# Kernel optimization log

Measured on AMD Instinct MI355X. Metric: run time of the kernel, lower is better.

## Reference

```python
import jax, jax.numpy as jnp
import numpy as np

N_NODES = 50000
N_EDGES = 600000
N_ELEMENTS = 100
N_RBF = 50
D = 128
CUTOFF = 5.0


def setup_inputs() -> dict:
    key = jax.random.key(0)
    ks = jax.random.split(key, 10)
    node_type = jax.random.randint(ks[0], (N_NODES,), 0, N_ELEMENTS)
    x_nodes = jax.random.normal(ks[1], (N_NODES, D), dtype=jnp.float32)
    src = jax.random.randint(ks[2], (N_EDGES,), 0, N_NODES)
    dst = jax.random.randint(ks[3], (N_EDGES,), 0, N_NODES)
    rbf_edges = jax.random.normal(ks[4], (N_EDGES, N_RBF), dtype=jnp.float32)
    dist = jax.random.uniform(ks[5], (N_EDGES,), dtype=jnp.float32) * (CUTOFF * 1.2)
    emb = jax.random.normal(ks[6], (N_ELEMENTS, D), dtype=jnp.float32) * 0.1
    W_e = jax.random.normal(ks[7], (D, N_RBF), dtype=jnp.float32) * (1.0 / np.sqrt(N_RBF))
    b_e = jnp.zeros((D,), dtype=jnp.float32)
    W_c = jax.random.normal(ks[8], (D, 2 * D), dtype=jnp.float32) * (1.0 / np.sqrt(2 * D))
    b_c = jnp.zeros((D,), dtype=jnp.float32)
    return {"node_type": node_type, "x_nodes": x_nodes, "src": src, "dst": dst,
            "rbf_edges": rbf_edges, "dist": dist, "emb": emb,
            "W_e": W_e, "b_e": b_e, "W_c": W_c, "b_c": b_c}


def cosine_cutoff(dist, cutoff):
    # 0.5*(cos(pi*d/cutoff)+1), zeroed beyond cutoff
    w = 0.5 * (jnp.cos(dist * (jnp.pi / cutoff)) + 1.0)
    return w * (dist < cutoff).astype(dist.dtype)


def reference(node_type, x_nodes, src, dst, rbf_edges, dist, emb, W_e, b_e, W_c, b_c):
    # node embedding from atom type: [N, D]
    x_neighbors = emb[node_type]
    # edge projection weighted by cutoff: [E, D]
    x_edges = (rbf_edges @ W_e.T + b_e) * cosine_cutoff(dist, CUTOFF)[:, None]
    # gather source node embedding, multiply by edge embedding, scatter-sum to dst
    msg = x_neighbors[src] * x_edges  # [E, D]
    x_integrated = jax.ops.segment_sum(msg, dst, num_segments=N_NODES)  # [N, D]
    # concat + combine linear: [N, D]
    x_combine = jnp.concatenate([x_nodes, x_integrated], axis=-1)
    return x_combine @ W_c.T + b_c
```

## Files before the change

kernel.cpp:

```cpp
#include <hip/hip_runtime.h>
#include <hip/hip_bf16.h>

constexpr int NN   = 50000;
constexpr int NE   = 600000;
constexpr int NRBF = 50;
constexpr int DIM  = 128;
constexpr float CUT = 5.0f;
constexpr float PI_F = 3.14159265358979323846f;

constexpr int CAP = 32;

constexpr size_t OFF_DEG   = 0;
constexpr size_t OFF_OVFC  = (size_t)NN * 4;
constexpr size_t OFF_EID   = 200960;
constexpr size_t OFF_OVF   = OFF_EID  + (size_t)NN * CAP * 4;
constexpr size_t OFF_CC    = OFF_OVF  + (size_t)NE * 4;
constexpr size_t OFF_EROW  = OFF_CC   + (size_t)NE * 4;
constexpr size_t OFF_WAUG  = OFF_EROW + (size_t)NE * 4;
constexpr size_t OFF_EPERM = OFF_WAUG + 128 * 64 * 2;
constexpr size_t OFF_MSG   = 13843200;
constexpr size_t OFF_XI    = OFF_MSG  + (size_t)NE * DIM * 2;


typedef __attribute__((ext_vector_type(4))) float f32x4;
typedef __attribute__((ext_vector_type(8))) short short8;

__device__ __forceinline__ float bf2f(unsigned short u) {
    return __uint_as_float(((unsigned int)u) << 16);
}
__device__ __forceinline__ unsigned short f2bf(float f) {
    return __bfloat16_as_ushort(__float2bfloat16(f));
}

__global__ __launch_bounds__(256)
void prep_w(const float* __restrict__ W_e, const float* __restrict__ b_e,
            const float* __restrict__ emb,
            unsigned short* __restrict__ W_aug, unsigned short* __restrict__ emb_perm)
{
    const int tid = blockIdx.x * 256 + threadIdx.x;
    if (tid < 128 * 64) {
        const int d = tid >> 6, k = tid & 63;
        float v = 0.0f;
        if (k < NRBF)       v = W_e[d * NRBF + k];
        else if (k == NRBF) v = b_e[d];
        W_aug[tid] = f2bf(v);
    } else if (tid < 128 * 64 + 100 * 128) {
        const int i = tid - 128 * 64;
        const int tau = i >> 7, p = i & 127;
        const int d = 16 * (p & 7) + (p >> 3);
        emb_perm[i] = f2bf(emb[tau * DIM + d]);
    }
}

__global__ __launch_bounds__(256)
void build_buckets(const int* __restrict__ dst, const float* __restrict__ dist,
                   const int* __restrict__ src, const int* __restrict__ node_type,
                   int* __restrict__ deg, int* __restrict__ eid,
                   int* __restrict__ ovf, int* __restrict__ ovf_cnt,
                   float* __restrict__ cc_arr, int* __restrict__ embrow)
{
    const int e = blockIdx.x * 256 + threadIdx.x;
    if (e >= NE) return;
    const float dd = dist[e];
    const bool act = dd < CUT;
    const float w = 0.5f * (__cosf(dd * (PI_F / CUT)) + 1.0f);
    cc_arr[e] = act ? w : 0.0f;
    embrow[e] = act ? node_type[src[e]] : -1;
    if (act) {
        const int n = dst[e];
        const int pos = atomicAdd(&deg[n], 1);
        if (pos < CAP) eid[n * CAP + pos] = e;
        else           ovf[atomicAdd(ovf_cnt, 1)] = e;
    }
}

__global__ __launch_bounds__(256)
void edge_msg_reg(const float* __restrict__ rbf,
                  const float* __restrict__ cc_arr,
                  const int* __restrict__ embrow,
                  const unsigned short* __restrict__ W_aug,
                  const unsigned short* __restrict__ emb_perm,
                  unsigned short* __restrict__ msg)
{
    const int t  = threadIdx.x;
    const int wv = t >> 6, l = t & 63;
    const int c  = l & 15, g = l >> 4;

    short8 bfrag[16];
    #pragma unroll
    for (int nt = 0; nt < 8; ++nt)
        #pragma unroll
        for (int s = 0; s < 2; ++s)
            bfrag[nt * 2 + s] =
                *(const short8*)(W_aug + (nt * 16 + c) * 64 + s * 32 + g * 8);

    #pragma unroll
    for (int tile = 0; tile < 4; ++tile) {
        const int e0 = (blockIdx.x * 4 + tile) * 64;
        if (e0 < NE) {
            const int er = e0 + wv * 16 + c;
            const float ccl = cc_arr[er];
            const float* rp = rbf + (size_t)er * NRBF;

            int erow[4];
            #pragma unroll
            for (int r = 0; r < 4; ++r)
                erow[r] = embrow[e0 + wv * 16 + 4 * g + r];

            const float2 r0 = *(const float2*)(rp + 8 * g);
            const float2 r1 = *(const float2*)(rp + 8 * g + 2);
            const float2 r2 = *(const float2*)(rp + 8 * g + 4);
            const float2 r3 = *(const float2*)(rp + 8 * g + 6);
            float2 q0 = make_float2(0.f, 0.f), q1 = q0, q2 = q0, q3 = q0;
            if (g < 2) {
                q0 = *(const float2*)(rp + 32 + 8 * g);
                q1 = *(const float2*)(rp + 32 + 8 * g + 2);
                q2 = *(const float2*)(rp + 32 + 8 * g + 4);
                q3 = *(const float2*)(rp + 32 + 8 * g + 6);
            } else if (g == 2) {
                q0 = *(const float2*)(rp + 48);
            }

            short8 a0, a1;
            a0[0] = (short)f2bf(ccl * r0.x); a0[1] = (short)f2bf(ccl * r0.y);
            a0[2] = (short)f2bf(ccl * r1.x); a0[3] = (short)f2bf(ccl * r1.y);
            a0[4] = (short)f2bf(ccl * r2.x); a0[5] = (short)f2bf(ccl * r2.y);
            a0[6] = (short)f2bf(ccl * r3.x); a0[7] = (short)f2bf(ccl * r3.y);
            a1[0] = (short)f2bf(ccl * q0.x); a1[1] = (short)f2bf(ccl * q0.y);
            a1[2] = (short)f2bf(ccl * q1.x); a1[3] = (short)f2bf(ccl * q1.y);
            a1[4] = (short)f2bf(ccl * q2.x); a1[5] = (short)f2bf(ccl * q2.y);
            a1[6] = (short)f2bf(ccl * q3.x); a1[7] = (short)f2bf(ccl * q3.y);
            if (g == 2) {
                a1[2] = (short)f2bf(ccl);
                a1[3] = 0; a1[4] = 0; a1[5] = 0; a1[6] = 0; a1[7] = 0;
            }

            f32x4 acc[8] = {};
            #pragma unroll
            for (int nt = 0; nt < 8; ++nt)
                acc[nt] = __builtin_amdgcn_mfma_f32_16x16x32_bf16(a0, bfrag[nt * 2],
                                                                  acc[nt], 0, 0, 0);
            #pragma unroll
            for (int nt = 0; nt < 8; ++nt)
                acc[nt] = __builtin_amdgcn_mfma_f32_16x16x32_bf16(a1, bfrag[nt * 2 + 1],
                                                                  acc[nt], 0, 0, 0);

            #pragma unroll
            for (int r = 0; r < 4; ++r) {
                const int e = e0 + wv * 16 + 4 * g + r;
                const int rw = erow[r];
                if (rw >= 0) {
                    const int4 em = *(const int4*)(emb_perm + rw * DIM + 8 * c);
                    const unsigned int* ep = (const unsigned int*)&em;
                    unsigned int ow[4];
                    #pragma unroll
                    for (int q = 0; q < 4; ++q) {
                        const float m0 = bf2f((unsigned short)(ep[q] & 0xffff));
                        const float m1 = bf2f((unsigned short)(ep[q] >> 16));
                        const float v0 = acc[2 * q][r] * m0;
                        const float v1 = acc[2 * q + 1][r] * m1;
                        ow[q] = (unsigned int)f2bf(v0) | ((unsigned int)f2bf(v1) << 16);
                    }
                    *(int4*)(msg + (size_t)e * DIM + 8 * c) =
                        make_int4((int)ow[0], (int)ow[1], (int)ow[2], (int)ow[3]);
                }
            }
        }
    }
}

__global__ __launch_bounds__(256)
void gather_sum(const unsigned short* __restrict__ msg, const int* __restrict__ deg,
                const int* __restrict__ eid, const int* __restrict__ ovf,
                const int* __restrict__ ovf_cnt, const int* __restrict__ dst,
                unsigned short* __restrict__ xi)
{
    const int t = threadIdx.x, l = t & 63;
    const int c = l & 15, g = l >> 4;
    const int n = blockIdx.x * 4 + (t >> 6);
    if (n >= NN) return;

    const int dn   = deg[n];
    const int degn = dn < CAP ? dn : CAP;
    int eidv = 0;
    if (l < degn) eidv = eid[n * CAP + l];

    float v[8] = {};
    for (int j = 0; j < degn; j += 4) {
        const int e = __shfl(eidv, j + g);
        if (j + g < degn) {
            const int4 mv = *(const int4*)(msg + (size_t)e * DIM + 8 * c);
            const unsigned int* mp = (const unsigned int*)&mv;
            #pragma unroll
            for (int q = 0; q < 4; ++q) {
                v[2 * q]     += bf2f((unsigned short)(mp[q] & 0xffff));
                v[2 * q + 1] += bf2f((unsigned short)(mp[q] >> 16));
            }
        }
    }
    const int ocnt = ovf_cnt[0];
    for (int j = 0; j < ocnt; ++j) {
        const int e = ovf[j];
        if (g == 0 && dst[e] == n) {
            const int4 mv = *(const int4*)(msg + (size_t)e * DIM + 8 * c);
            const unsigned int* mp = (const unsigned int*)&mv;
            #pragma unroll
            for (int q = 0; q < 4; ++q) {
                v[2 * q]     += bf2f((unsigned short)(mp[q] & 0xffff));
                v[2 * q + 1] += bf2f((unsigned short)(mp[q] >> 16));
            }
        }
    }

    #pragma unroll
    for (int q = 0; q < 8; ++q) {
        v[q] += __shfl_xor(v[q], 16);
        v[q] += __shfl_xor(v[q], 32);
    }

    float s0 = v[0], s1 = v[1];
    if (g == 1)      { s0 = v[2]; s1 = v[3]; }
    else if (g == 2) { s0 = v[4]; s1 = v[5]; }
    else if (g == 3) { s0 = v[6]; s1 = v[7]; }
    xi[(size_t)n * DIM + 32 * g + c]      = f2bf(s0);
    xi[(size_t)n * DIM + 32 * g + 16 + c] = f2bf(s1);
}

__global__ __launch_bounds__(256)
void combine_mfma(const float* __restrict__ x_nodes, const __hip_bfloat16* __restrict__ xi,
                  const float* __restrict__ W_c, const float* __restrict__ b_c,
                  float* __restrict__ out)
{
    __shared__ unsigned short As[64][72];
    __shared__ unsigned short Bs[128][72];

    const int t  = threadIdx.x;
    const int wv = t >> 6;
    const int l  = t & 63;
    const int n0 = blockIdx.x * 64;

    f32x4 acc[8] = {};

    for (int kc = 0; kc < 4; ++kc) {
        const int kb = kc * 64;
        if (kc) __syncthreads();
        {
            const int r  = t >> 2;
            const int c0 = (t & 3) * 16;
            const int n  = n0 + r;
            if (kc < 2) {
                float4 v[4];
                if (n < NN) {
                    const float4* p = (const float4*)(x_nodes + (size_t)n * DIM + kb + c0);
                    v[0] = p[0]; v[1] = p[1]; v[2] = p[2]; v[3] = p[3];
                } else {
                    v[0] = v[1] = v[2] = v[3] = make_float4(0.f, 0.f, 0.f, 0.f);
                }
                unsigned short* dp = &As[r][c0];
                #pragma unroll
                for (int q = 0; q < 4; ++q) {
                    *(ushort2*)&dp[q * 4]     = make_ushort2(f2bf(v[q].x), f2bf(v[q].y));
                    *(ushort2*)&dp[q * 4 + 2] = make_ushort2(f2bf(v[q].z), f2bf(v[q].w));
                }
            } else {
                int4 v0 = make_int4(0, 0, 0, 0), v1 = make_int4(0, 0, 0, 0);
                if (n < NN) {
                    const int4* p = (const int4*)(xi + (size_t)n * DIM + (kb - DIM) + c0);
                    v0 = p[0];
                    v1 = p[1];
                }
                *(int4*)&As[r][c0]     = v0;
                *(int4*)&As[r][c0 + 8] = v1;
            }
        }
        {
            const int dch = t >> 1;
            const int c0  = (t & 1) * 32;
            const float4* p = (const float4*)(W_c + (size_t)dch * (2 * DIM) + kb + c0);
            unsigned short* dp = &Bs[dch][c0];
            #pragma unroll
            for (int q = 0; q < 8; ++q) {
                const float4 v = p[q];
                *(ushort2*)&dp[q * 4]     = make_ushort2(f2bf(v.x), f2bf(v.y));
                *(ushort2*)&dp[q * 4 + 2] = make_ushort2(f2bf(v.z), f2bf(v.w));
            }
        }
        __syncthreads();
        #pragma unroll
        for (int s = 0; s < 2; ++s) {
            const int ko = s * 32 + (l >> 4) * 8;
            const short8 af = *(const short8*)&As[wv * 16 + (l & 15)][ko];
            #pragma unroll
            for (int nt = 0; nt < 8; ++nt) {
                const short8 bf = *(const short8*)&Bs[nt * 16 + (l & 15)][ko];
                acc[nt] = __builtin_amdgcn_mfma_f32_16x16x32_bf16(af, bf, acc[nt], 0, 0, 0);
            }
        }
    }

    const int col = l & 15;
    const int rq  = (l >> 4) * 4;
    #pragma unroll
    for (int nt = 0; nt < 8; ++nt) {
        const int dim = nt * 16 + col;
        const float bc = b_c[dim];
        #pragma unroll
        for (int r = 0; r < 4; ++r) {
            const int node = n0 + wv * 16 + rq + r;
            if (node < NN)
                out[(size_t)node * DIM + dim] = acc[nt][r] + bc;
        }
    }
}

extern "C" void kernel_launch(void* const* d_in, const int* in_sizes, int n_in,
                              void* d_out, int out_size, void* d_ws, size_t ws_size,
                              hipStream_t stream)
{
    const int*   node_type = (const int*)  d_in[0];
    const float* x_nodes   = (const float*)d_in[1];
    const int*   src       = (const int*)  d_in[2];
    const int*   dst       = (const int*)  d_in[3];
    const float* rbf       = (const float*)d_in[4];
    const float* dist      = (const float*)d_in[5];
    const float* emb       = (const float*)d_in[6];
    const float* W_e       = (const float*)d_in[7];
    const float* b_e       = (const float*)d_in[8];
    const float* W_c       = (const float*)d_in[9];
    const float* b_c       = (const float*)d_in[10];
    float* out = (float*)d_out;

    char* ws = (char*)d_ws;
    int*            deg      = (int*)(ws + OFF_DEG);
    int*            ovf_cnt  = (int*)(ws + OFF_OVFC);
    int*            eid      = (int*)(ws + OFF_EID);
    int*            ovf      = (int*)(ws + OFF_OVF);
    float*          cc_arr   = (float*)(ws + OFF_CC);
    int*            embrow   = (int*)(ws + OFF_EROW);
    unsigned short* W_aug    = (unsigned short*)(ws + OFF_WAUG);
    unsigned short* emb_perm = (unsigned short*)(ws + OFF_EPERM);
    unsigned short* msg      = (unsigned short*)(ws + OFF_MSG);
    unsigned short* xi       = (unsigned short*)(ws + OFF_XI);

    hipMemsetAsync(deg, 0, (NN + 1) * sizeof(int), stream);

    prep_w<<<82, 256, 0, stream>>>(W_e, b_e, emb, W_aug, emb_perm);

    build_buckets<<<(NE + 255) / 256, 256, 0, stream>>>(
        dst, dist, src, node_type, deg, eid, ovf, ovf_cnt, cc_arr, embrow);

    edge_msg_reg<<<(NE / 64 + 3) / 4, 256, 0, stream>>>(
        rbf, cc_arr, embrow, W_aug, emb_perm, msg);

    gather_sum<<<(NN + 3) / 4, 256, 0, stream>>>(msg, deg, eid, ovf, ovf_cnt, dst, xi);

    combine_mfma<<<(NN + 63) / 64, 256, 0, stream>>>(
        x_nodes, (const __hip_bfloat16*)xi, W_c, b_c, out);
}
```

Before: 356.9 us.

## Double-buffer rbf tiles into LDS via async global_load_lds in edge kernel

```diff
diff --git a/kernel.cpp b/kernel.cpp
--- a/kernel.cpp
+++ b/kernel.cpp
@@ -9,6 +9,7 @@
 constexpr float PI_F = 3.14159265358979323846f;
 
 constexpr int CAP = 32;
+constexpr int NTILES = NE / 64;
 
 constexpr size_t OFF_DEG   = 0;
 constexpr size_t OFF_OVFC  = (size_t)NN * 4;
@@ -74,14 +75,32 @@
     }
 }
 
-__global__ __launch_bounds__(256)
-void edge_msg_reg(const float* __restrict__ rbf,
+__device__ __forceinline__ void stage_rbf(const float* __restrict__ rbf, int tt,
+                                          void* lds_base, int wv, int l)
+{
+    const char* gb = (const char*)rbf + (size_t)tt * 12800 + (size_t)wv * 3200;
+    char* lb = (char*)lds_base + wv * 3200;
+    #pragma unroll
+    for (int i = 0; i < 4; ++i) {
+        if (i * 64 + l < 200) {
+            __builtin_amdgcn_global_load_lds(
+                (const __attribute__((address_space(1))) unsigned int*)(gb + (size_t)(i * 64 + l) * 16),
+                (__attribute__((address_space(3))) unsigned int*)(lb + i * 1024),
+                16, 0, 0);
+        }
+    }
+}
+
+__global__ __launch_bounds__(256)
+void edge_msg_lds(const float* __restrict__ rbf,
                   const float* __restrict__ cc_arr,
                   const int* __restrict__ embrow,
                   const unsigned short* __restrict__ W_aug,
                   const unsigned short* __restrict__ emb_perm,
                   unsigned short* __restrict__ msg)
 {
+    __shared__ __align__(16) float sbuf[2][3200];
+
     const int t  = threadIdx.x;
     const int wv = t >> 6, l = t & 63;
     const int c  = l & 15, g = l >> 4;
@@ -94,31 +113,43 @@
             bfrag[nt * 2 + s] =
                 *(const short8*)(W_aug + (nt * 16 + c) * 64 + s * 32 + g * 8);
 
+    const int tt0 = blockIdx.x * 4;
+
+    stage_rbf(rbf, tt0, (void*)sbuf[0], wv, l);
+
     #pragma unroll
     for (int tile = 0; tile < 4; ++tile) {
-        const int e0 = (blockIdx.x * 4 + tile) * 64;
-        if (e0 < NE) {
+        const int tt = tt0 + tile;
+
+        if (tile < 3 && tt + 1 < NTILES) {
+            stage_rbf(rbf, tt + 1, (void*)sbuf[(tile + 1) & 1], wv, l);
+            asm volatile("s_waitcnt vmcnt(4)" ::: "memory");
+        } else {
+            asm volatile("s_waitcnt vmcnt(0)" ::: "memory");
+        }
+
+        if (tt < NTILES) {
+            const int e0 = tt * 64;
             const int er = e0 + wv * 16 + c;
             const float ccl = cc_arr[er];
-            const float* rp = rbf + (size_t)er * NRBF;
-
-            int erow[4];
-            #pragma unroll
-            for (int r = 0; r < 4; ++r)
-                erow[r] = embrow[e0 + wv * 16 + 4 * g + r];
-
-            const float2 r0 = *(const float2*)(rp + 8 * g);
-            const float2 r1 = *(const float2*)(rp + 8 * g + 2);
-            const float2 r2 = *(const float2*)(rp + 8 * g + 4);
-            const float2 r3 = *(const float2*)(rp + 8 * g + 6);
+
+            const int4 er4 = *(const int4*)(embrow + e0 + wv * 16 + 4 * g);
+            const int* erow = (const int*)&er4;
+
+            const float2* rp2 =
+                (const float2*)((const char*)sbuf[tile & 1] + (wv * 16 + c) * 200);
+            const float2 r0 = rp2[4 * g];
+            const float2 r1 = rp2[4 * g + 1];
+            const float2 r2 = rp2[4 * g + 2];
+            const float2 r3 = rp2[4 * g + 3];
             float2 q0 = make_float2(0.f, 0.f), q1 = q0, q2 = q0, q3 = q0;
             if (g < 2) {
-                q0 = *(const float2*)(rp + 32 + 8 * g);
-                q1 = *(const float2*)(rp + 32 + 8 * g + 2);
-                q2 = *(const float2*)(rp + 32 + 8 * g + 4);
-                q3 = *(const float2*)(rp + 32 + 8 * g + 6);
+                q0 = rp2[16 + 4 * g];
+                q1 = rp2[17 + 4 * g];
+                q2 = rp2[18 + 4 * g];
+                q3 = rp2[19 + 4 * g];
             } else if (g == 2) {
-                q0 = *(const float2*)(rp + 48);
+                q0 = rp2[24];
             }
 
             short8 a0, a1;
@@ -349,7 +380,7 @@
     build_buckets<<<(NE + 255) / 256, 256, 0, stream>>>(
         dst, dist, src, node_type, deg, eid, ovf, ovf_cnt, cc_arr, embrow);
 
-    edge_msg_reg<<<(NE / 64 + 3) / 4, 256, 0, stream>>>(
+    edge_msg_lds<<<(NTILES + 3) / 4, 256, 0, stream>>>(
         rbf, cc_arr, embrow, W_aug, emb_perm, msg);
 
     gather_sum<<<(NN + 3) / 4, 256, 0, stream>>>(msg, deg, eid, ovf, ovf_cnt, dst, xi);
```

Result: no change. 356.5 us (-0.1%).

## Fuse edge message MFMA into per-destination gather, dropping the msg buffer

Applied to the files above, without the earlier changes.

```diff
diff --git a/kernel.cpp b/kernel.cpp
--- a/kernel.cpp
+++ b/kernel.cpp
@@ -13,13 +13,12 @@
 constexpr size_t OFF_DEG   = 0;
 constexpr size_t OFF_OVFC  = (size_t)NN * 4;
 constexpr size_t OFF_EID   = 200960;
-constexpr size_t OFF_OVF   = OFF_EID  + (size_t)NN * CAP * 4;
-constexpr size_t OFF_CC    = OFF_OVF  + (size_t)NE * 4;
-constexpr size_t OFF_EROW  = OFF_CC   + (size_t)NE * 4;
-constexpr size_t OFF_WAUG  = OFF_EROW + (size_t)NE * 4;
+constexpr size_t OFF_CCB   = OFF_EID  + (size_t)NN * CAP * 4;
+constexpr size_t OFF_TAUB  = OFF_CCB  + (size_t)NN * CAP * 4;
+constexpr size_t OFF_OVF   = OFF_TAUB + (size_t)NN * CAP * 4;
+constexpr size_t OFF_WAUG  = OFF_OVF  + (size_t)NE * 4;
 constexpr size_t OFF_EPERM = OFF_WAUG + 128 * 64 * 2;
-constexpr size_t OFF_MSG   = 13843200;
-constexpr size_t OFF_XI    = OFF_MSG  + (size_t)NE * DIM * 2;
+constexpr size_t OFF_XI    = OFF_EPERM + 100 * 128 * 2;
 
 
 typedef __attribute__((ext_vector_type(4))) float f32x4;
@@ -56,158 +55,139 @@
 void build_buckets(const int* __restrict__ dst, const float* __restrict__ dist,
                    const int* __restrict__ src, const int* __restrict__ node_type,
                    int* __restrict__ deg, int* __restrict__ eid,
-                   int* __restrict__ ovf, int* __restrict__ ovf_cnt,
-                   float* __restrict__ cc_arr, int* __restrict__ embrow)
+                   float* __restrict__ ccb, int* __restrict__ taub,
+                   int* __restrict__ ovf, int* __restrict__ ovf_cnt)
 {
     const int e = blockIdx.x * 256 + threadIdx.x;
     if (e >= NE) return;
     const float dd = dist[e];
-    const bool act = dd < CUT;
+    if (dd >= CUT) return;
     const float w = 0.5f * (__cosf(dd * (PI_F / CUT)) + 1.0f);
-    cc_arr[e] = act ? w : 0.0f;
-    embrow[e] = act ? node_type[src[e]] : -1;
-    if (act) {
-        const int n = dst[e];
-        const int pos = atomicAdd(&deg[n], 1);
-        if (pos < CAP) eid[n * CAP + pos] = e;
-        else           ovf[atomicAdd(ovf_cnt, 1)] = e;
+    const int n = dst[e];
+    const int pos = atomicAdd(&deg[n], 1);
+    if (pos < CAP) {
+        eid[n * CAP + pos]  = e;
+        ccb[n * CAP + pos]  = w;
+        taub[n * CAP + pos] = node_type[src[e]];
+    } else {
+        ovf[atomicAdd(ovf_cnt, 1)] = e;
     }
 }
 
 __global__ __launch_bounds__(256)
-void edge_msg_reg(const float* __restrict__ rbf,
-                  const float* __restrict__ cc_arr,
-                  const int* __restrict__ embrow,
+void gather_fused(const float* __restrict__ rbf,
+                  const int* __restrict__ deg, const int* __restrict__ eid,
+                  const float* __restrict__ ccb, const int* __restrict__ taub,
                   const unsigned short* __restrict__ W_aug,
                   const unsigned short* __restrict__ emb_perm,
-                  unsigned short* __restrict__ msg)
-{
-    const int t  = threadIdx.x;
-    const int wv = t >> 6, l = t & 63;
-    const int c  = l & 15, g = l >> 4;
-
-    short8 bfrag[16];
-    #pragma unroll
-    for (int nt = 0; nt < 8; ++nt)
-        #pragma unroll
-        for (int s = 0; s < 2; ++s)
-            bfrag[nt * 2 + s] =
-                *(const short8*)(W_aug + (nt * 16 + c) * 64 + s * 32 + g * 8);
-
-    #pragma unroll
-    for (int tile = 0; tile < 4; ++tile) {
-        const int e0 = (blockIdx.x * 4 + tile) * 64;
-        if (e0 < NE) {
-            const int er = e0 + wv * 16 + c;
-            const float ccl = cc_arr[er];
-            const float* rp = rbf + (size_t)er * NRBF;
-
-            int erow[4];
-            #pragma unroll
-            for (int r = 0; r < 4; ++r)
-                erow[r] = embrow[e0 + wv * 16 + 4 * g + r];
-
-            const float2 r0 = *(const float2*)(rp + 8 * g);
-            const float2 r1 = *(const float2*)(rp + 8 * g + 2);
-            const float2 r2 = *(const float2*)(rp + 8 * g + 4);
-            const float2 r3 = *(const float2*)(rp + 8 * g + 6);
-            float2 q0 = make_float2(0.f, 0.f), q1 = q0, q2 = q0, q3 = q0;
-            if (g < 2) {
-                q0 = *(const float2*)(rp + 32 + 8 * g);
-                q1 = *(const float2*)(rp + 32 + 8 * g + 2);
-                q2 = *(const float2*)(rp + 32 + 8 * g + 4);
-                q3 = *(const float2*)(rp + 32 + 8 * g + 6);
-            } else if (g == 2) {
-                q0 = *(const float2*)(rp + 48);
-            }
-
-            short8 a0, a1;
-            a0[0] = (short)f2bf(ccl * r0.x); a0[1] = (short)f2bf(ccl * r0.y);
-            a0[2] = (short)f2bf(ccl * r1.x); a0[3] = (short)f2bf(ccl * r1.y);
-            a0[4] = (short)f2bf(ccl * r2.x); a0[5] = (short)f2bf(ccl * r2.y);
-            a0[6] = (short)f2bf(ccl * r3.x); a0[7] = (short)f2bf(ccl * r3.y);
-            a1[0] = (short)f2bf(ccl * q0.x); a1[1] = (short)f2bf(ccl * q0.y);
-            a1[2] = (short)f2bf(ccl * q1.x); a1[3] = (short)f2bf(ccl * q1.y);
-            a1[4] = (short)f2bf(ccl * q2.x); a1[5] = (short)f2bf(ccl * q2.y);
-            a1[6] = (short)f2bf(ccl * q3.x); a1[7] = (short)f2bf(ccl * q3.y);
-            if (g == 2) {
-                a1[2] = (short)f2bf(ccl);
-                a1[3] = 0; a1[4] = 0; a1[5] = 0; a1[6] = 0; a1[7] = 0;
-            }
-
-            f32x4 acc[8] = {};
-            #pragma unroll
-            for (int nt = 0; nt < 8; ++nt)
-                acc[nt] = __builtin_amdgcn_mfma_f32_16x16x32_bf16(a0, bfrag[nt * 2],
-                                                                  acc[nt], 0, 0, 0);
-            #pragma unroll
-            for (int nt = 0; nt < 8; ++nt)
-                acc[nt] = __builtin_amdgcn_mfma_f32_16x16x32_bf16(a1, bfrag[nt * 2 + 1],
-                                                                  acc[nt], 0, 0, 0);
-
-            #pragma unroll
-            for (int r = 0; r < 4; ++r) {
-                const int e = e0 + wv * 16 + 4 * g + r;
-                const int rw = erow[r];
-                if (rw >= 0) {
-                    const int4 em = *(const int4*)(emb_perm + rw * DIM + 8 * c);
-                    const unsigned int* ep = (const unsigned int*)&em;
-                    unsigned int ow[4];
-                    #pragma unroll
-                    for (int q = 0; q < 4; ++q) {
-                        const float m0 = bf2f((unsigned short)(ep[q] & 0xffff));
-                        const float m1 = bf2f((unsigned short)(ep[q] >> 16));
-                        const float v0 = acc[2 * q][r] * m0;
-                        const float v1 = acc[2 * q + 1][r] * m1;
-                        ow[q] = (unsigned int)f2bf(v0) | ((unsigned int)f2bf(v1) << 16);
-                    }
-                    *(int4*)(msg + (size_t)e * DIM + 8 * c) =
-                        make_int4((int)ow[0], (int)ow[1], (int)ow[2], (int)ow[3]);
-                }
-            }
-        }
-    }
-}
-
-__global__ __launch_bounds__(256)
-void gather_sum(const unsigned short* __restrict__ msg, const int* __restrict__ deg,
-                const int* __restrict__ eid, const int* __restrict__ ovf,
-                const int* __restrict__ ovf_cnt, const int* __restrict__ dst,
-                unsigned short* __restrict__ xi)
+                  const int* __restrict__ ovf, const int* __restrict__ ovf_cnt,
+                  const int* __restrict__ dst, const float* __restrict__ dist,
+                  const int* __restrict__ src, const int* __restrict__ node_type,
+                  unsigned short* __restrict__ xi)
 {
     const int t = threadIdx.x, l = t & 63;
     const int c = l & 15, g = l >> 4;
     const int n = blockIdx.x * 4 + (t >> 6);
     if (n >= NN) return;
 
+    short8 bfrag[16];
+    #pragma unroll
+    for (int nt = 0; nt < 8; ++nt)
+        #pragma unroll
+        for (int s = 0; s < 2; ++s)
+            bfrag[nt * 2 + s] =
+                *(const short8*)(W_aug + (nt * 16 + c) * 64 + s * 32 + g * 8);
+
     const int dn   = deg[n];
     const int degn = dn < CAP ? dn : CAP;
-    int eidv = 0;
-    if (l < degn) eidv = eid[n * CAP + l];
+    const int base = n * CAP;
 
     float v[8] = {};
-    for (int j = 0; j < degn; j += 4) {
-        const int e = __shfl(eidv, j + g);
-        if (j + g < degn) {
-            const int4 mv = *(const int4*)(msg + (size_t)e * DIM + 8 * c);
-            const unsigned int* mp = (const unsigned int*)&mv;
-            #pragma unroll
-            for (int q = 0; q < 4; ++q) {
-                v[2 * q]     += bf2f((unsigned short)(mp[q] & 0xffff));
-                v[2 * q + 1] += bf2f((unsigned short)(mp[q] >> 16));
-            }
-        }
-    }
+
+    for (int j0 = 0; j0 < degn; j0 += 16) {
+        const int slot = j0 + c;
+        int   ea  = 0;
+        float ccl = 0.0f;
+        if (slot < degn) {
+            ea  = eid[base + slot];
+            ccl = ccb[base + slot];
+        }
+        const float* rp = rbf + (size_t)ea * NRBF;
+
+        const float2* rp2 = (const float2*)rp;
+        const float2 r0 = rp2[4 * g];
+        const float2 r1 = rp2[4 * g + 1];
+        const float2 r2 = rp2[4 * g + 2];
+        const float2 r3 = rp2[4 * g + 3];
+        float2 q0 = make_float2(0.f, 0.f), q1 = q0, q2 = q0, q3 = q0;
+        if (g < 2) {
+            q0 = rp2[16 + 4 * g];
+            q1 = rp2[17 + 4 * g];
+            q2 = rp2[18 + 4 * g];
+            q3 = rp2[19 + 4 * g];
+        } else if (g == 2) {
+            q0 = rp2[24];
+        }
+
+        short8 a0, a1;
+        a0[0] = (short)f2bf(ccl * r0.x); a0[1] = (short)f2bf(ccl * r0.y);
+        a0[2] = (short)f2bf(ccl * r1.x); a0[3] = (short)f2bf(ccl * r1.y);
+        a0[4] = (short)f2bf(ccl * r2.x); a0[5] = (short)f2bf(ccl * r2.y);
+        a0[6] = (short)f2bf(ccl * r3.x); a0[7] = (short)f2bf(ccl * r3.y);
+        a1[0] = (short)f2bf(ccl * q0.x); a1[1] = (short)f2bf(ccl * q0.y);
+        a1[2] = (short)f2bf(ccl * q1.x); a1[3] = (short)f2bf(ccl * q1.y);
+        a1[4] = (short)f2bf(ccl * q2.x); a1[5] = (short)f2bf(ccl * q2.y);
+        a1[6] = (short)f2bf(ccl * q3.x); a1[7] = (short)f2bf(ccl * q3.y);
+        if (g == 2) {
+            a1[2] = (short)f2bf(ccl);
+            a1[3] = 0; a1[4] = 0; a1[5] = 0; a1[6] = 0; a1[7] = 0;
+        }
+
+        f32x4 acc[8] = {};
+        #pragma unroll
+        for (int nt = 0; nt < 8; ++nt)
+            acc[nt] = __builtin_amdgcn_mfma_f32_16x16x32_bf16(a0, bfrag[nt * 2],
+                                                              acc[nt], 0, 0, 0);
+        #pragma unroll
+        for (int nt = 0; nt < 8; ++nt)
+            acc[nt] = __builtin_amdgcn_mfma_f32_16x16x32_bf16(a1, bfrag[nt * 2 + 1],
+                                                              acc[nt], 0, 0, 0);
+
+        #pragma unroll
+        for (int r = 0; r < 4; ++r) {
+            const int jr = j0 + 4 * g + r;
+            if (jr < degn) {
+                const int rw = taub[base + jr];
+                const int4 em = *(const int4*)(emb_perm + rw * DIM + 8 * c);
+                const unsigned int* ep = (const unsigned int*)&em;
+                #pragma unroll
+                for (int q = 0; q < 4; ++q) {
+                    const float m0 = bf2f((unsigned short)(ep[q] & 0xffff));
+                    const float m1 = bf2f((unsigned short)(ep[q] >> 16));
+                    v[2 * q]     += bf2f(f2bf(acc[2 * q][r]     * m0));
+                    v[2 * q + 1] += bf2f(f2bf(acc[2 * q + 1][r] * m1));
+                }
+            }
+        }
+    }
+
     const int ocnt = ovf_cnt[0];
     for (int j = 0; j < ocnt; ++j) {
         const int e = ovf[j];
-        if (g == 0 && dst[e] == n) {
-            const int4 mv = *(const int4*)(msg + (size_t)e * DIM + 8 * c);
-            const unsigned int* mp = (const unsigned int*)&mv;
+        if (dst[e] != n) continue;
+        const float dd  = dist[e];
+        const float ccl = 0.5f * (__cosf(dd * (PI_F / CUT)) + 1.0f);
+        if (g == 0) {
+            const int tau = node_type[src[e]];
+            const float* rp = rbf + (size_t)e * NRBF;
+            const float ccb16 = bf2f(f2bf(ccl));
             #pragma unroll
-            for (int q = 0; q < 4; ++q) {
-                v[2 * q]     += bf2f((unsigned short)(mp[q] & 0xffff));
-                v[2 * q + 1] += bf2f((unsigned short)(mp[q] >> 16));
+            for (int q = 0; q < 8; ++q) {
+                const int d = 16 * q + c;
+                float s = bf2f(W_aug[d * 64 + NRBF]) * ccb16;
+                for (int k = 0; k < NRBF; ++k)
+                    s += bf2f(W_aug[d * 64 + k]) * bf2f(f2bf(ccl * rp[k]));
+                v[q] += bf2f(f2bf(s * bf2f(emb_perm[tau * DIM + 8 * c + q])));
             }
         }
     }
@@ -334,12 +314,11 @@
     int*            deg      = (int*)(ws + OFF_DEG);
     int*            ovf_cnt  = (int*)(ws + OFF_OVFC);
     int*            eid      = (int*)(ws + OFF_EID);
+    float*          ccb      = (float*)(ws + OFF_CCB);
+    int*            taub     = (int*)(ws + OFF_TAUB);
     int*            ovf      = (int*)(ws + OFF_OVF);
-    float*          cc_arr   = (float*)(ws + OFF_CC);
-    int*            embrow   = (int*)(ws + OFF_EROW);
     unsigned short* W_aug    = (unsigned short*)(ws + OFF_WAUG);
     unsigned short* emb_perm = (unsigned short*)(ws + OFF_EPERM);
-    unsigned short* msg      = (unsigned short*)(ws + OFF_MSG);
     unsigned short* xi       = (unsigned short*)(ws + OFF_XI);
 
     hipMemsetAsync(deg, 0, (NN + 1) * sizeof(int), stream);
@@ -347,12 +326,11 @@
     prep_w<<<82, 256, 0, stream>>>(W_e, b_e, emb, W_aug, emb_perm);
 
     build_buckets<<<(NE + 255) / 256, 256, 0, stream>>>(
-        dst, dist, src, node_type, deg, eid, ovf, ovf_cnt, cc_arr, embrow);
-
-    edge_msg_reg<<<(NE / 64 + 3) / 4, 256, 0, stream>>>(
-        rbf, cc_arr, embrow, W_aug, emb_perm, msg);
-
-    gather_sum<<<(NN + 3) / 4, 256, 0, stream>>>(msg, deg, eid, ovf, ovf_cnt, dst, xi);
+        dst, dist, src, node_type, deg, eid, ccb, taub, ovf, ovf_cnt);
+
+    gather_fused<<<(NN + 3) / 4, 256, 0, stream>>>(
+        rbf, deg, eid, ccb, taub, W_aug, emb_perm,
+        ovf, ovf_cnt, dst, dist, src, node_type, xi);
 
     combine_mfma<<<(NN + 63) / 64, 256, 0, stream>>>(
         x_nodes, (const __hip_bfloat16*)xi, W_c, b_c, out);
```

After: 454.0 us. 27.2% more time.
